# Performance work log

Measured on AMD Instinct MI355X. Metric: run time of the kernel, lower is better.

Reference implementation:

```python
import jax, jax.numpy as jnp
import numpy as np

MP_TIMES = 3  # mp_times from init


def setup_inputs() -> dict:
    key = jax.random.key(0)
    ks = jax.random.split(key, 16)
    N, E, F, EF = 10000, 50000, 32, 16
    DL, D, G, GD, OUT = 128, 64, 256, 8, 1

    def w(k, shape, fan_in):
        return jax.random.normal(k, shape, jnp.float32) / np.float32(np.sqrt(fan_in))

    return {
        "x": jax.random.normal(ks[0], (N, F), jnp.float32),
        "edge_index": jax.random.randint(ks[1], (2, E), 0, N),
        "edge_attr": jax.random.uniform(ks[2], (E, EF), jnp.float32),
        "batch": jax.random.randint(ks[3], (N,), 0, G),
        "graph_attr": jax.random.normal(ks[4], (G, GD), jnp.float32),
        # lin0
        "W0": w(ks[5], (D, F), F), "b0": jnp.zeros((D,), jnp.float32),
        # edge network MLP: EF -> DL -> D*D
        "We1": w(ks[6], (DL, EF), EF), "be1": jnp.zeros((DL,), jnp.float32),
        "We2": w(ks[7], (D * D, DL), DL), "be2": jnp.zeros((D * D,), jnp.float32),
        # NNConv root weight + bias
        "Wroot": w(ks[8], (D, D), D), "bconv": jnp.zeros((D,), jnp.float32),
        # GRU (torch gate order: r, z, n)
        "W_ih": w(ks[9], (3 * D, D), D), "W_hh": w(ks[10], (3 * D, D), D),
        "b_ih": jnp.zeros((3 * D,), jnp.float32), "b_hh": jnp.zeros((3 * D,), jnp.float32),
        # lin1 takes cat(node_state, graph_attr) -> D  (sized D+GD to make the source's cat runnable)
        "W1": w(ks[11], (D, D + GD), D + GD), "b1": jnp.zeros((D,), jnp.float32),
        # lin2
        "W2": w(ks[12], (OUT, D), D), "b2": jnp.zeros((OUT,), jnp.float32),
    }


def reference(x, edge_index, edge_attr, batch, graph_attr,
              W0, b0, We1, be1, We2, be2, Wroot, bconv,
              W_ih, W_hh, b_ih, b_hh, W1, b1, W2, b2):
    N = x.shape[0]
    D = W0.shape[0]
    src, dst = edge_index[0], edge_index[1]

    # Per-edge weight matrices from the edge MLP (loop-invariant: edge_attr is constant).
    ew = jnp.maximum(edge_attr @ We1.T + be1, 0.0) @ We2.T + be2  # [E, D*D]
    ew = ew.reshape(-1, D, D)                                      # [E, D, D]

    # mean-aggregation denominator (isolated nodes keep 0 via max(deg,1))
    deg = jax.ops.segment_sum(jnp.ones(src.shape[0], jnp.float32), dst, num_segments=N)
    denom = jnp.maximum(deg, 1.0)[:, None]                         # [N, 1]

    out = jnp.maximum(x @ W0.T + b0, 0.0)                          # [N, D]
    h = out
    for _ in range(MP_TIMES):
        # NNConv: gather -> per-edge matmul -> scatter-mean, plus root transform
        msg = jnp.einsum('ei,eio->eo', out[src], ew)               # [E, D]
        agg = jax.ops.segment_sum(msg, dst, num_segments=N) / denom
        m = jnp.maximum(agg + out @ Wroot.T + bconv, 0.0)          # [N, D]
        # single GRU step (torch GRUCell math, gate order r,z,n)
        gi = m @ W_ih.T + b_ih
        gh = h @ W_hh.T + b_hh
        i_r, i_z, i_n = jnp.split(gi, 3, axis=-1)
        h_r, h_z, h_n = jnp.split(gh, 3, axis=-1)
        r = jax.nn.sigmoid(i_r + h_r)
        z = jax.nn.sigmoid(i_z + h_z)
        n = jnp.tanh(i_n + r * h_n)
        h = (1.0 - z) * n + z * h
        out = h

    cat = jnp.concatenate([out, graph_attr[batch]], axis=-1)       # [N, D+GD]
    hid = jnp.maximum(cat @ W1.T + b1, 0.0)
    return hid @ W2.T + b2                                         # [N, dim_output]
```

## Files before the change

kernel.cpp:

```cpp
#include <hip/hip_runtime.h>
#include <hip/hip_bf16.h>
#include <math.h>

#define FIN 32
#define EFD 16
#define GDIM 8
#define ISPLIT 2

typedef __attribute__((ext_vector_type(8))) short short8;
typedef __attribute__((ext_vector_type(4))) float f32x4;

static __device__ __forceinline__ float bf2f(unsigned short u) {
  return __uint_as_float(((unsigned)u) << 16);
}
static __device__ __forceinline__ unsigned short f2bf(float f) {
  unsigned u = __float_as_uint(f);
  unsigned r = (u + 0x7FFFu + ((u >> 16) & 1u)) >> 16;
  return (unsigned short)r;
}

__global__ void zero_f32(float* __restrict__ p, int n) {
  int i = blockIdx.x * blockDim.x + threadIdx.x;
  if (i < n) p[i] = 0.0f;
}

__global__ void deg_kernel(const int* __restrict__ dst, float* __restrict__ deg, int E) {
  int e = blockIdx.x * blockDim.x + threadIdx.x;
  if (e < E) atomicAdd(&deg[dst[e]], 1.0f);
}

__global__ void setup_fused(const float* __restrict__ ea, const float* __restrict__ We1,
                            const float* __restrict__ be1, unsigned short* __restrict__ hidden,
                            const float* __restrict__ We2, unsigned short* __restrict__ We2f,
                            const float* __restrict__ Wroot, const float* __restrict__ W_hh,
                            const float* __restrict__ be2, const float* __restrict__ W_ih,
                            unsigned short* __restrict__ Wc_fh, unsigned short* __restrict__ Wc_fl,
                            unsigned short* __restrict__ Wih_fh, unsigned short* __restrict__ Wih_fl,
                            const float* __restrict__ x, const float* __restrict__ W0,
                            const float* __restrict__ b0, float* __restrict__ state,
                            int E, int N, int eB, int cB, int pB) {
  int b = blockIdx.x;
  if (b < eB) {
    int idx = b * 256 + threadIdx.x;
    int e = idx >> 7, l = idx & 127;
    if (e >= E) return;
    float acc = be1[l];
    const float* er = ea + (size_t)e * EFD;
    const float* wr = We1 + (size_t)l * EFD;
    #pragma unroll
    for (int j = 0; j < EFD; ++j) acc += er[j] * wr[j];
    hidden[idx] = f2bf(fmaxf(acc, 0.0f));
    return;
  }
  b -= eB;
  if (b < cB) {
    int fidx = b * 256 + threadIdx.x;
    if (fidx >= 4096 * 128) return;
    int j    = fidx & 7;
    int lane = (fidx >> 3) & 63;
    int kk   = (fidx >> 9) & 3;
    int wave = (fidx >> 11) & 3;
    int i    = fidx >> 13;
    int quad = lane >> 4, col = lane & 15;
    int row  = i * 64 + wave * 16 + col;
    int cw   = kk * 32 + quad * 8 + j;
    We2f[fidx] = f2bf(We2[(size_t)row * 128 + cw]);
    return;
  }
  b -= cB;
  if (b < pB) {
    int idx = b * 256 + threadIdx.x;
    if (idx >= 20480 + 12288) return;
    if (idx < 20480) {
      int j = idx & 7, lane = (idx >> 3) & 63, kk = (idx >> 9) & 1, cgk = idx >> 10;
      int quad = lane >> 4, mcol = lane & 15;
      int wave = cgk / 5, cg = cgk % 5;
      int c = wave * 80 + cg * 16 + mcol;
      int cw = kk * 32 + quad * 8 + j;
      float w;
      if (c < 64)       w = Wroot[c * 64 + cw];
      else if (c < 256) w = W_hh[(c - 64) * 64 + cw];
      else              w = be2[cw * 64 + (c - 256)];
      unsigned short h = f2bf(w);
      Wc_fh[idx] = h;
      Wc_fl[idx] = f2bf(w - bf2f(h));
    } else {
      int t = idx - 20480;
      int j = t & 7, lane = (t >> 3) & 63, kk = (t >> 9) & 1, gw = t >> 10;
      int quad = lane >> 4, mcol = lane & 15;
      int g = gw >> 2, wave = gw & 3;
      int row = g * 64 + wave * 16 + mcol;
      int cw = kk * 32 + quad * 8 + j;
      float w = W_ih[row * 64 + cw];
      unsigned short h = f2bf(w);
      Wih_fh[t] = h;
      Wih_fl[t] = f2bf(w - bf2f(h));
    }
    return;
  }
  b -= pB;
  {
    int idx = b * 256 + threadIdx.x;
    int n = idx >> 6, d = idx & 63;
    if (n >= N) return;
    float acc = b0[d];
    const float* xr = x + (size_t)n * FIN;
    const float* wr = W0 + (size_t)d * FIN;
    #pragma unroll
    for (int f = 0; f < FIN; ++f) acc += xr[f] * wr[f];
    state[idx] = fmaxf(acc, 0.0f);
  }
}

#define MFMA(A, B, C) __builtin_amdgcn_mfma_f32_16x16x32_bf16((A), (B), (C), 0, 0, 0)

__global__ __launch_bounds__(256) void pre_kernel(const float* __restrict__ state,
    const unsigned short* __restrict__ Wc_fh, const unsigned short* __restrict__ Wc_fl,
    float* __restrict__ R, int N) {
  __shared__ __align__(16) unsigned short Sh[32 * 72], Sl[32 * 72];
  int tid = threadIdx.x;
  int n0 = blockIdx.x * 32;
  {
    int nl = tid >> 3, part = tid & 7;
    int gn = n0 + nl;
    const float* sp = state + (size_t)gn * 64 + part * 8;
    #pragma unroll
    for (int j = 0; j < 2; ++j) {
      float4 v = make_float4(0.f, 0.f, 0.f, 0.f);
      if (gn < N) v = *(const float4*)(sp + j * 4);
      int base = nl * 72 + part * 8 + j * 4;
      unsigned short h;
      h = f2bf(v.x); Sh[base + 0] = h; Sl[base + 0] = f2bf(v.x - bf2f(h));
      h = f2bf(v.y); Sh[base + 1] = h; Sl[base + 1] = f2bf(v.y - bf2f(h));
      h = f2bf(v.z); Sh[base + 2] = h; Sl[base + 2] = f2bf(v.z - bf2f(h));
      h = f2bf(v.w); Sh[base + 3] = h; Sl[base + 3] = f2bf(v.w - bf2f(h));
    }
  }
  __syncthreads();
  int lane = tid & 63, wave = tid >> 6;
  int quad = lane >> 4, mcol = lane & 15;
  short8 ah[2][2], al[2][2];
  #pragma unroll
  for (int mt = 0; mt < 2; ++mt)
    #pragma unroll
    for (int kk = 0; kk < 2; ++kk) {
      ah[mt][kk] = *(const short8*)&Sh[(mt * 16 + mcol) * 72 + kk * 32 + quad * 8];
      al[mt][kk] = *(const short8*)&Sl[(mt * 16 + mcol) * 72 + kk * 32 + quad * 8];
    }
  int c0w = wave * 80;
  #pragma unroll 1
  for (int cg = 0; cg < 5; ++cg) {
    int c = c0w + cg * 16 + mcol;
    const unsigned short* bhp = Wc_fh + (size_t)(wave * 5 + cg) * 1024 + lane * 8;
    const unsigned short* blp = Wc_fl + (size_t)(wave * 5 + cg) * 1024 + lane * 8;
    short8 bh0 = *(const short8*)bhp, bh1 = *(const short8*)(bhp + 512);
    short8 bl0 = *(const short8*)blp, bl1 = *(const short8*)(blp + 512);
    #pragma unroll
    for (int mt = 0; mt < 2; ++mt) {
      f32x4 p = (f32x4){0.f, 0.f, 0.f, 0.f};
      p = MFMA(al[mt][0], bh0, p);
      p = MFMA(ah[mt][0], bl0, p);
      p = MFMA(ah[mt][0], bh0, p);
      p = MFMA(al[mt][1], bh1, p);
      p = MFMA(ah[mt][1], bl1, p);
      p = MFMA(ah[mt][1], bh1, p);
      #pragma unroll
      for (int r = 0; r < 4; ++r) {
        int row = n0 + mt * 16 + quad * 4 + r;
        if (row < N) R[(size_t)row * 320 + c] = p[r];
      }
    }
  }
}

__global__ __launch_bounds__(256) void msg_fused(const int* __restrict__ ei,
    const float* __restrict__ state, const unsigned short* __restrict__ hidden,
    const unsigned short* __restrict__ We2f, const float* __restrict__ R,
    float* __restrict__ agg, int E) {
  __shared__ __align__(16) char smem[64 * 136 * 2];
  __shared__ int srcs[64], dsts[64];
  unsigned short* Hs = (unsigned short*)smem;
  float* St = (float*)smem;
  int tid = threadIdx.x;
  int e0 = blockIdx.x * 64;
  int i0 = blockIdx.y * 32;
  if (tid < 64) {
    int e = e0 + tid;
    srcs[tid] = (e < E) ? ei[e] : -1;
    dsts[tid] = (e < E) ? ei[E + e] : -1;
  }
  {
    int er = tid >> 2, part = tid & 3;
    int ge = e0 + er;
    const unsigned short* hp = hidden + (size_t)ge * 128 + part * 32;
    #pragma unroll
    for (int j = 0; j < 4; ++j) {
      uint4 v = make_uint4(0u, 0u, 0u, 0u);
      if (ge < E) v = *(const uint4*)(hp + j * 8);
      *(uint4*)&Hs[er * 136 + part * 32 + j * 8] = v;
    }
  }
  __syncthreads();
  int lane = tid & 63, wave = tid >> 6;
  int n0 = wave * 16;
  int quad = lane >> 4, col = lane & 15;
  short8 a[4][4];
  #pragma unroll
  for (int mt = 0; mt < 4; ++mt)
    #pragma unroll
    for (int kk = 0; kk < 4; ++kk)
      a[mt][kk] = *(const short8*)&Hs[(mt * 16 + col) * 136 + kk * 32 + quad * 8];
  float4 sreg[2];
  {
    int sn = srcs[lane];
    const float* sp = state + (size_t)(sn < 0 ? 0 : sn) * 64 + i0 + wave * 8;
    #pragma unroll
    for (int j = 0; j < 2; ++j) {
      float4 v = make_float4(0.f, 0.f, 0.f, 0.f);
      if (sn >= 0) v = *(const float4*)(sp + j * 4);
      sreg[j] = v;
    }
  }
  __syncthreads();
  #pragma unroll
  for (int j = 0; j < 2; ++j) {
    int i = wave * 8 + j * 4;
    St[(i + 0) * 64 + lane] = sreg[j].x;
    St[(i + 1) * 64 + lane] = sreg[j].y;
    St[(i + 2) * 64 + lane] = sreg[j].z;
    St[(i + 3) * 64 + lane] = sreg[j].w;
  }
  __syncthreads();

  f32x4 macc0 = (f32x4){0.f,0.f,0.f,0.f}, macc1 = (f32x4){0.f,0.f,0.f,0.f};
  f32x4 macc2 = (f32x4){0.f,0.f,0.f,0.f}, macc3 = (f32x4){0.f,0.f,0.f,0.f};
  const unsigned short* bptr = We2f + (size_t)i0 * 8192 + wave * 2048 + lane * 8;
  short8 Xa = *(const short8*)(bptr + 0);
  short8 Xb = *(const short8*)(bptr + 512);
  short8 Xc = *(const short8*)(bptr + 1024);
  short8 Xd = *(const short8*)(bptr + 1536);
  short8 Ya, Yb, Yc, Yd;
  #pragma unroll 1
  for (int ii = 0; ii < 16; ++ii) {
    int i = ii * 2;
    {
      const unsigned short* bn = bptr + (size_t)(i + 1) * 8192;
      Ya = *(const short8*)(bn + 0);
      Yb = *(const short8*)(bn + 512);
      Yc = *(const short8*)(bn + 1024);
      Yd = *(const short8*)(bn + 1536);
    }
    {
      f32x4 sv0 = *(const f32x4*)&St[i * 64 +  0 + quad * 4];
      f32x4 sv1 = *(const f32x4*)&St[i * 64 + 16 + quad * 4];
      f32x4 sv2 = *(const f32x4*)&St[i * 64 + 32 + quad * 4];
      f32x4 sv3 = *(const f32x4*)&St[i * 64 + 48 + quad * 4];
      f32x4 p0 = (f32x4){0.f,0.f,0.f,0.f}, p1 = (f32x4){0.f,0.f,0.f,0.f};
      f32x4 p2 = (f32x4){0.f,0.f,0.f,0.f}, p3 = (f32x4){0.f,0.f,0.f,0.f};
      p0 = MFMA(a[0][0], Xa, p0); p1 = MFMA(a[1][0], Xa, p1);
      p2 = MFMA(a[2][0], Xa, p2); p3 = MFMA(a[3][0], Xa, p3);
      p0 = MFMA(a[0][1], Xb, p0); p1 = MFMA(a[1][1], Xb, p1);
      p2 = MFMA(a[2][1], Xb, p2); p3 = MFMA(a[3][1], Xb, p3);
      p0 = MFMA(a[0][2], Xc, p0); p1 = MFMA(a[1][2], Xc, p1);
      p2 = MFMA(a[2][2], Xc, p2); p3 = MFMA(a[3][2], Xc, p3);
      p0 = MFMA(a[0][3], Xd, p0); p1 = MFMA(a[1][3], Xd, p1);
      p2 = MFMA(a[2][3], Xd, p2); p3 = MFMA(a[3][3], Xd, p3);
      macc0 += sv0 * p0; macc1 += sv1 * p1; macc2 += sv2 * p2; macc3 += sv3 * p3;
    }
    if (ii < 15) {
      const unsigned short* bn = bptr + (size_t)(i + 2) * 8192;
      Xa = *(const short8*)(bn + 0);
      Xb = *(const short8*)(bn + 512);
      Xc = *(const short8*)(bn + 1024);
      Xd = *(const short8*)(bn + 1536);
    }
    {
      int io = i + 1;
      f32x4 sv0 = *(const f32x4*)&St[io * 64 +  0 + quad * 4];
      f32x4 sv1 = *(const f32x4*)&St[io * 64 + 16 + quad * 4];
      f32x4 sv2 = *(const f32x4*)&St[io * 64 + 32 + quad * 4];
      f32x4 sv3 = *(const f32x4*)&St[io * 64 + 48 + quad * 4];
      f32x4 p0 = (f32x4){0.f,0.f,0.f,0.f}, p1 = (f32x4){0.f,0.f,0.f,0.f};
      f32x4 p2 = (f32x4){0.f,0.f,0.f,0.f}, p3 = (f32x4){0.f,0.f,0.f,0.f};
      p0 = MFMA(a[0][0], Ya, p0); p1 = MFMA(a[1][0], Ya, p1);
      p2 = MFMA(a[2][0], Ya, p2); p3 = MFMA(a[3][0], Ya, p3);
      p0 = MFMA(a[0][1], Yb, p0); p1 = MFMA(a[1][1], Yb, p1);
      p2 = MFMA(a[2][1], Yb, p2); p3 = MFMA(a[3][1], Yb, p3);
      p0 = MFMA(a[0][2], Yc, p0); p1 = MFMA(a[1][2], Yc, p1);
      p2 = MFMA(a[2][2], Yc, p2); p3 = MFMA(a[3][2], Yc, p3);
      p0 = MFMA(a[0][3], Yd, p0); p1 = MFMA(a[1][3], Yd, p1);
      p2 = MFMA(a[2][3], Yd, p2); p3 = MFMA(a[3][3], Yd, p3);
      macc0 += sv0 * p0; macc1 += sv1 * p1; macc2 += sv2 * p2; macc3 += sv3 * p3;
    }
  }
  int addu = (blockIdx.y == 0);
  f32x4 maccA[4] = {macc0, macc1, macc2, macc3};
  #pragma unroll
  for (int mt = 0; mt < 4; ++mt) {
    #pragma unroll
    for (int r = 0; r < 4; ++r) {
      int el = mt * 16 + quad * 4 + r;
      int d = dsts[el];
      if (d >= 0) {
        float val = maccA[mt][r];
        if (addu) val += R[(size_t)srcs[el] * 320 + 256 + n0 + col];
        atomicAdd(&agg[(size_t)d * 64 + n0 + col], val);
      }
    }
  }
}

__global__ __launch_bounds__(256) void gate_pre(float* __restrict__ agg,
    const float* __restrict__ deg, float* __restrict__ state,
    float* __restrict__ R, const float* __restrict__ bconv,
    const unsigned short* __restrict__ Wih_fh, const unsigned short* __restrict__ Wih_fl,
    const float* __restrict__ b_ih, const float* __restrict__ b_hh,
    const unsigned short* __restrict__ Wc_fh, const unsigned short* __restrict__ Wc_fl,
    int N, int do_pre) {
  __shared__ __align__(16) unsigned short Mh[16 * 72], Ml[16 * 72];
  int tid = threadIdx.x;
  int n0 = blockIdx.x * 16;
  {
    int nl = tid >> 4, part = tid & 15;
    int gn = n0 + nl;
    float inv = 1.0f;
    if (gn < N) inv = 1.0f / fmaxf(deg[gn], 1.0f);
    int o = part * 4;
    float4 av = make_float4(0.f, 0.f, 0.f, 0.f);
    float4 rv = make_float4(0.f, 0.f, 0.f, 0.f);
    if (gn < N) {
      av = *(const float4*)(agg + (size_t)gn * 64 + o);
      rv = *(const float4*)(R + (size_t)gn * 320 + o);
    }
    float4 bv = *(const float4*)(bconv + o);
    float m0 = fmaxf(av.x * inv + rv.x + bv.x, 0.0f);
    float m1 = fmaxf(av.y * inv + rv.y + bv.y, 0.0f);
    float m2 = fmaxf(av.z * inv + rv.z + bv.z, 0.0f);
    float m3 = fmaxf(av.w * inv + rv.w + bv.w, 0.0f);
    int base = nl * 72 + o;
    unsigned short h;
    h = f2bf(m0); Mh[base + 0] = h; Ml[base + 0] = f2bf(m0 - bf2f(h));
    h = f2bf(m1); Mh[base + 1] = h; Ml[base + 1] = f2bf(m1 - bf2f(h));
    h = f2bf(m2); Mh[base + 2] = h; Ml[base + 2] = f2bf(m2 - bf2f(h));
    h = f2bf(m3); Mh[base + 3] = h; Ml[base + 3] = f2bf(m3 - bf2f(h));
    if (gn < N)
      *(float4*)(agg + (size_t)gn * 64 + o) = make_float4(0.f, 0.f, 0.f, 0.f);
  }
  __syncthreads();
  int lane = tid & 63, wave = tid >> 6;
  int quad = lane >> 4, mcol = lane & 15;
  short8 ah[2], al[2];
  #pragma unroll
  for (int kk = 0; kk < 2; ++kk) {
    ah[kk] = *(const short8*)&Mh[mcol * 72 + kk * 32 + quad * 8];
    al[kk] = *(const short8*)&Ml[mcol * 72 + kk * 32 + quad * 8];
  }
  int c = wave * 16 + mcol;
  f32x4 accg[3];
  #pragma unroll 1
  for (int g = 0; g < 3; ++g) {
    const unsigned short* bhp = Wih_fh + (size_t)g * 4096 + wave * 1024 + lane * 8;
    const unsigned short* blp = Wih_fl + (size_t)g * 4096 + wave * 1024 + lane * 8;
    short8 bh0 = *(const short8*)bhp, bh1 = *(const short8*)(bhp + 512);
    short8 bl0 = *(const short8*)blp, bl1 = *(const short8*)(blp + 512);
    f32x4 p = (f32x4){0.f, 0.f, 0.f, 0.f};
    p = MFMA(al[0], bh0, p);
    p = MFMA(ah[0], bl0, p);
    p = MFMA(ah[0], bh0, p);
    p = MFMA(al[1], bh1, p);
    p = MFMA(ah[1], bl1, p);
    p = MFMA(ah[1], bh1, p);
    accg[g] = p;
  }
  float bir = b_ih[c], biz = b_ih[64 + c], bin = b_ih[128 + c];
  float bhr = b_hh[c], bhz = b_hh[64 + c], bhn = b_hh[128 + c];
  float hnew[4];
  #pragma unroll
  for (int r = 0; r < 4; ++r) {
    int node = n0 + quad * 4 + r;
    hnew[r] = 0.0f;
    if (node >= N) continue;
    const float* Rn = R + (size_t)node * 320;
    float gir = accg[0][r] + bir + Rn[64 + c] + bhr;
    float giz = accg[1][r] + biz + Rn[128 + c] + bhz;
    float ghn = Rn[192 + c] + bhn;
    float rg = 1.0f / (1.0f + expf(-gir));
    float zg = 1.0f / (1.0f + expf(-giz));
    float ng = tanhf(accg[2][r] + bin + rg * ghn);
    size_t si = (size_t)node * 64 + c;
    float h = state[si];
    float hv = (1.0f - zg) * ng + zg * h;
    state[si] = hv;
    hnew[r] = hv;
  }
  if (!do_pre) return;
  __syncthreads();
  #pragma unroll
  for (int r = 0; r < 4; ++r) {
    int base = (quad * 4 + r) * 72 + c;
    float v = hnew[r];
    unsigned short h = f2bf(v);
    Mh[base] = h; Ml[base] = f2bf(v - bf2f(h));
  }
  __syncthreads();
  short8 ph[2], pl[2];
  #pragma unroll
  for (int kk = 0; kk < 2; ++kk) {
    ph[kk] = *(const short8*)&Mh[mcol * 72 + kk * 32 + quad * 8];
    pl[kk] = *(const short8*)&Ml[mcol * 72 + kk * 32 + quad * 8];
  }
  #pragma unroll 1
  for (int cg = 0; cg < 5; ++cg) {
    int cc = wave * 80 + cg * 16 + mcol;
    const unsigned short* bhp = Wc_fh + (size_t)(wave * 5 + cg) * 1024 + lane * 8;
    const unsigned short* blp = Wc_fl + (size_t)(wave * 5 + cg) * 1024 + lane * 8;
    short8 bh0 = *(const short8*)bhp, bh1 = *(const short8*)(bhp + 512);
    short8 bl0 = *(const short8*)blp, bl1 = *(const short8*)(blp + 512);
    f32x4 p = (f32x4){0.f, 0.f, 0.f, 0.f};
    p = MFMA(pl[0], bh0, p);
    p = MFMA(ph[0], bl0, p);
    p = MFMA(ph[0], bh0, p);
    p = MFMA(pl[1], bh1, p);
    p = MFMA(ph[1], bl1, p);
    p = MFMA(ph[1], bh1, p);
    #pragma unroll
    for (int r = 0; r < 4; ++r) {
      int row = n0 + quad * 4 + r;
      if (row < N) R[(size_t)row * 320 + cc] = p[r];
    }
  }
}

__global__ __launch_bounds__(256) void final_kernel(const float* __restrict__ state,
    const int* __restrict__ batch, const float* __restrict__ gattr,
    const float* __restrict__ W1, const float* __restrict__ b1,
    const float* __restrict__ W2, const float* __restrict__ b2,
    float* __restrict__ out, int N) {
  int lane = threadIdx.x & 63;
  int n = blockIdx.x * 4 + (threadIdx.x >> 6);
  if (n >= N) return;
  float s = state[(size_t)n * 64 + lane];
  int b = batch[n];
  float acc = b1[lane];
  const float* w = W1 + (size_t)lane * 72;
  for (int i = 0; i < 64; ++i) acc += __shfl(s, i) * w[i];
  const float* gar = gattr + (size_t)b * GDIM;
  #pragma unroll
  for (int j = 0; j < GDIM; ++j) acc += gar[j] * w[64 + j];
  float hid = fmaxf(acc, 0.0f);
  float v = hid * W2[lane];
  #pragma unroll
  for (int off = 32; off > 0; off >>= 1) v += __shfl_xor(v, off);
  if (lane == 0) out[n] = v + b2[0];
}

extern "C" void kernel_launch(void* const* d_in, const int* in_sizes, int n_in,
                              void* d_out, int out_size, void* d_ws, size_t ws_size,
                              hipStream_t stream) {
  const float* x     = (const float*)d_in[0];
  const int*   ei    = (const int*)d_in[1];
  const float* ea    = (const float*)d_in[2];
  const int*   batch = (const int*)d_in[3];
  const float* ga    = (const float*)d_in[4];
  const float* W0    = (const float*)d_in[5];
  const float* b0    = (const float*)d_in[6];
  const float* We1   = (const float*)d_in[7];
  const float* be1   = (const float*)d_in[8];
  const float* We2   = (const float*)d_in[9];
  const float* be2   = (const float*)d_in[10];
  const float* Wroot = (const float*)d_in[11];
  const float* bconv = (const float*)d_in[12];
  const float* W_ih  = (const float*)d_in[13];
  const float* W_hh  = (const float*)d_in[14];
  const float* b_ih  = (const float*)d_in[15];
  const float* b_hh  = (const float*)d_in[16];
  const float* W1    = (const float*)d_in[17];
  const float* b1    = (const float*)d_in[18];
  const float* W2    = (const float*)d_in[19];
  const float* b2    = (const float*)d_in[20];
  int N = in_sizes[0] / FIN;
  int E = in_sizes[1] / 2;
  float* out = (float*)d_out;

  char* p = (char*)d_ws;
  float* state = (float*)p; p += (size_t)N * 64 * 4;
  float* agg   = (float*)p; p += (size_t)N * 64 * 4;
  float* deg   = (float*)p; p += ((size_t)N * 4 + 15) & ~(size_t)15;
  float* R     = (float*)p; p += (size_t)N * 320 * 4;
  unsigned short* hidden = (unsigned short*)p; p += (size_t)E * 128 * 2;
  unsigned short* We2f   = (unsigned short*)p; p += (size_t)4096 * 128 * 2;
  unsigned short* Wc_fh  = (unsigned short*)p; p += 320 * 64 * 2;
  unsigned short* Wc_fl  = (unsigned short*)p; p += 320 * 64 * 2;
  unsigned short* Wih_fh = (unsigned short*)p; p += 192 * 64 * 2;
  unsigned short* Wih_fl = (unsigned short*)p; p += 192 * 64 * 2;

  int tileBlocks32 = (N + 31) / 32;
  int tileBlocks16 = (N + 15) / 16;
  int edgeBlocks = (E + 63) / 64;

  int eB = (E * 128 + 255) / 256;
  int cB = (4096 * 128 + 255) / 256;
  int pB = (32768 + 255) / 256;
  int lB = (N * 64 + 255) / 256;

  zero_f32<<<(N * 65 + 255) / 256, 256, 0, stream>>>(agg, N * 65);
  deg_kernel<<<(E + 255) / 256, 256, 0, stream>>>(ei + E, deg, E);
  setup_fused<<<eB + cB + pB + lB, 256, 0, stream>>>(
      ea, We1, be1, hidden, We2, We2f, Wroot, W_hh, be2, W_ih,
      Wc_fh, Wc_fl, Wih_fh, Wih_fl, x, W0, b0, state, E, N, eB, cB, pB);
  pre_kernel<<<tileBlocks32, 256, 0, stream>>>(state, Wc_fh, Wc_fl, R, N);
  for (int t = 0; t < 3; ++t) {
    dim3 mg(edgeBlocks, ISPLIT);
    msg_fused<<<mg, 256, 0, stream>>>(ei, state, hidden, We2f, R, agg, E);
    gate_pre<<<tileBlocks16, 256, 0, stream>>>(agg, deg, state, R, bconv,
                                               Wih_fh, Wih_fl, b_ih, b_hh,
                                               Wc_fh, Wc_fl, N, (t < 2) ? 1 : 0);
  }
  final_kernel<<<(N + 3) / 4, 256, 0, stream>>>(state, batch, ga, W1, b1, W2, b2, out, N);
}
```

Before: 409.5 us.

## Split bias-term scatter into separate blocks and fuse final MLP into last gate kernel

The per-edge addition of the R[src] slice (the extra column block at offset 256) moves out of the MFMA message blocks into extra lightweight blocks in the same launch, one wave per edge, each doing a coalesced 64-lane atomic scatter. The 2D grid is flattened to 1D. The final readout MLP (lin1 + lin2) is folded into the last gate_pre launch, which removes one kernel launch and a re-read of state. The price is more atomic traffic, since the bias term now gets its own atomics per edge, and a serial per-wave loop over 4 nodes in the fused tail.

```diff
diff --git a/kernel.cpp b/kernel.cpp
--- a/kernel.cpp
+++ b/kernel.cpp
@@ -176,18 +176,32 @@
 __global__ __launch_bounds__(256) void msg_fused(const int* __restrict__ ei,
     const float* __restrict__ state, const unsigned short* __restrict__ hidden,
     const unsigned short* __restrict__ We2f, const float* __restrict__ R,
-    float* __restrict__ agg, int E) {
+    float* __restrict__ agg, int E, int edgeBlocks) {
+  int tid = threadIdx.x;
+  int lane = tid & 63, wave = tid >> 6;
+  int mb = edgeBlocks * ISPLIT;
+  if ((int)blockIdx.x >= mb) {
+    int e = (blockIdx.x - mb) * 4 + wave;
+    if (e < E) {
+      int src = ei[e], dst = ei[E + e];
+      float val = R[(size_t)src * 320 + 256 + lane];
+      atomicAdd(&agg[(size_t)dst * 64 + lane], val);
+    }
+    return;
+  }
   __shared__ __align__(16) char smem[64 * 136 * 2];
-  __shared__ int srcs[64], dsts[64];
+  __shared__ int dsts[64];
   unsigned short* Hs = (unsigned short*)smem;
   float* St = (float*)smem;
-  int tid = threadIdx.x;
-  int e0 = blockIdx.x * 64;
-  int i0 = blockIdx.y * 32;
-  if (tid < 64) {
-    int e = e0 + tid;
-    srcs[tid] = (e < E) ? ei[e] : -1;
-    dsts[tid] = (e < E) ? ei[E + e] : -1;
+  int by = blockIdx.x / edgeBlocks;
+  int bx = blockIdx.x % edgeBlocks;
+  int e0 = bx * 64;
+  int i0 = by * 32;
+  int snL;
+  {
+    int eL = e0 + lane;
+    snL = (eL < E) ? ei[eL] : -1;
+    if (tid < 64) dsts[tid] = (eL < E) ? ei[E + eL] : -1;
   }
   {
     int er = tid >> 2, part = tid & 3;
@@ -201,7 +215,6 @@
     }
   }
   __syncthreads();
-  int lane = tid & 63, wave = tid >> 6;
   int n0 = wave * 16;
   int quad = lane >> 4, col = lane & 15;
   short8 a[4][4];
@@ -212,12 +225,11 @@
       a[mt][kk] = *(const short8*)&Hs[(mt * 16 + col) * 136 + kk * 32 + quad * 8];
   float4 sreg[2];
   {
-    int sn = srcs[lane];
-    const float* sp = state + (size_t)(sn < 0 ? 0 : sn) * 64 + i0 + wave * 8;
+    const float* sp = state + (size_t)(snL < 0 ? 0 : snL) * 64 + i0 + wave * 8;
     #pragma unroll
     for (int j = 0; j < 2; ++j) {
       float4 v = make_float4(0.f, 0.f, 0.f, 0.f);
-      if (sn >= 0) v = *(const float4*)(sp + j * 4);
+      if (snL >= 0) v = *(const float4*)(sp + j * 4);
       sreg[j] = v;
     }
   }
@@ -293,7 +305,6 @@
       macc0 += sv0 * p0; macc1 += sv1 * p1; macc2 += sv2 * p2; macc3 += sv3 * p3;
     }
   }
-  int addu = (blockIdx.y == 0);
   f32x4 maccA[4] = {macc0, macc1, macc2, macc3};
   #pragma unroll
   for (int mt = 0; mt < 4; ++mt) {
@@ -301,11 +312,8 @@
     for (int r = 0; r < 4; ++r) {
       int el = mt * 16 + quad * 4 + r;
       int d = dsts[el];
-      if (d >= 0) {
-        float val = maccA[mt][r];
-        if (addu) val += R[(size_t)srcs[el] * 320 + 256 + n0 + col];
-        atomicAdd(&agg[(size_t)d * 64 + n0 + col], val);
-      }
+      if (d >= 0)
+        atomicAdd(&agg[(size_t)d * 64 + n0 + col], maccA[mt][r]);
     }
   }
 }
@@ -316,7 +324,10 @@
     const unsigned short* __restrict__ Wih_fh, const unsigned short* __restrict__ Wih_fl,
     const float* __restrict__ b_ih, const float* __restrict__ b_hh,
     const unsigned short* __restrict__ Wc_fh, const unsigned short* __restrict__ Wc_fl,
-    int N, int do_pre) {
+    const int* __restrict__ batch, const float* __restrict__ gattr,
+    const float* __restrict__ W1, const float* __restrict__ b1,
+    const float* __restrict__ W2, const float* __restrict__ b2,
+    float* __restrict__ out, int N, int do_pre) {
   __shared__ __align__(16) unsigned short Mh[16 * 72], Ml[16 * 72];
   int tid = threadIdx.x;
   int n0 = blockIdx.x * 16;
@@ -393,65 +404,69 @@
     state[si] = hv;
     hnew[r] = hv;
   }
-  if (!do_pre) return;
-  __syncthreads();
-  #pragma unroll
-  for (int r = 0; r < 4; ++r) {
-    int base = (quad * 4 + r) * 72 + c;
-    float v = hnew[r];
-    unsigned short h = f2bf(v);
-    Mh[base] = h; Ml[base] = f2bf(v - bf2f(h));
-  }
-  __syncthreads();
-  short8 ph[2], pl[2];
-  #pragma unroll
-  for (int kk = 0; kk < 2; ++kk) {
-    ph[kk] = *(const short8*)&Mh[mcol * 72 + kk * 32 + quad * 8];
-    pl[kk] = *(const short8*)&Ml[mcol * 72 + kk * 32 + quad * 8];
-  }
-  #pragma unroll 1
-  for (int cg = 0; cg < 5; ++cg) {
-    int cc = wave * 80 + cg * 16 + mcol;
-    const unsigned short* bhp = Wc_fh + (size_t)(wave * 5 + cg) * 1024 + lane * 8;
-    const unsigned short* blp = Wc_fl + (size_t)(wave * 5 + cg) * 1024 + lane * 8;
-    short8 bh0 = *(const short8*)bhp, bh1 = *(const short8*)(bhp + 512);
-    short8 bl0 = *(const short8*)blp, bl1 = *(const short8*)(blp + 512);
-    f32x4 p = (f32x4){0.f, 0.f, 0.f, 0.f};
-    p = MFMA(pl[0], bh0, p);
-    p = MFMA(ph[0], bl0, p);
-    p = MFMA(ph[0], bh0, p);
-    p = MFMA(pl[1], bh1, p);
-    p = MFMA(ph[1], bl1, p);
-    p = MFMA(ph[1], bh1, p);
+  if (do_pre) {
+    __syncthreads();
     #pragma unroll
     for (int r = 0; r < 4; ++r) {
-      int row = n0 + quad * 4 + r;
-      if (row < N) R[(size_t)row * 320 + cc] = p[r];
-    }
-  }
-}
-
-__global__ __launch_bounds__(256) void final_kernel(const float* __restrict__ state,
-    const int* __restrict__ batch, const float* __restrict__ gattr,
-    const float* __restrict__ W1, const float* __restrict__ b1,
-    const float* __restrict__ W2, const float* __restrict__ b2,
-    float* __restrict__ out, int N) {
-  int lane = threadIdx.x & 63;
-  int n = blockIdx.x * 4 + (threadIdx.x >> 6);
-  if (n >= N) return;
-  float s = state[(size_t)n * 64 + lane];
-  int b = batch[n];
-  float acc = b1[lane];
-  const float* w = W1 + (size_t)lane * 72;
-  for (int i = 0; i < 64; ++i) acc += __shfl(s, i) * w[i];
-  const float* gar = gattr + (size_t)b * GDIM;
-  #pragma unroll
-  for (int j = 0; j < GDIM; ++j) acc += gar[j] * w[64 + j];
-  float hid = fmaxf(acc, 0.0f);
-  float v = hid * W2[lane];
-  #pragma unroll
-  for (int off = 32; off > 0; off >>= 1) v += __shfl_xor(v, off);
-  if (lane == 0) out[n] = v + b2[0];
+      int base = (quad * 4 + r) * 72 + c;
+      float v = hnew[r];
+      unsigned short h = f2bf(v);
+      Mh[base] = h; Ml[base] = f2bf(v - bf2f(h));
+    }
+    __syncthreads();
+    short8 ph[2], pl[2];
+    #pragma unroll
+    for (int kk = 0; kk < 2; ++kk) {
+      ph[kk] = *(const short8*)&Mh[mcol * 72 + kk * 32 + quad * 8];
+      pl[kk] = *(const short8*)&Ml[mcol * 72 + kk * 32 + quad * 8];
+    }
+    #pragma unroll 1
+    for (int cg = 0; cg < 5; ++cg) {
+      int cc = wave * 80 + cg * 16 + mcol;
+      const unsigned short* bhp = Wc_fh + (size_t)(wave * 5 + cg) * 1024 + lane * 8;
+      const unsigned short* blp = Wc_fl + (size_t)(wave * 5 + cg) * 1024 + lane * 8;
+      short8 bh0 = *(const short8*)bhp, bh1 = *(const short8*)(bhp + 512);
+      short8 bl0 = *(const short8*)blp, bl1 = *(const short8*)(blp + 512);
+      f32x4 p = (f32x4){0.f, 0.f, 0.f, 0.f};
+      p = MFMA(pl[0], bh0, p);
+      p = MFMA(ph[0], bl0, p);
+      p = MFMA(ph[0], bh0, p);
+      p = MFMA(pl[1], bh1, p);
+      p = MFMA(ph[1], bl1, p);
+      p = MFMA(ph[1], bh1, p);
+      #pragma unroll
+      for (int r = 0; r < 4; ++r) {
+        int row = n0 + quad * 4 + r;
+        if (row < N) R[(size_t)row * 320 + cc] = p[r];
+      }
+    }
+  } else {
+    __syncthreads();
+    float* Hf = (float*)Mh;
+    #pragma unroll
+    for (int r = 0; r < 4; ++r)
+      Hf[(quad * 4 + r) * 64 + c] = hnew[r];
+    __syncthreads();
+    const float* w = W1 + (size_t)lane * 72;
+    #pragma unroll 1
+    for (int nl = 0; nl < 4; ++nl) {
+      int node_local = wave * 4 + nl;
+      int node = n0 + node_local;
+      if (node >= N) continue;
+      float s = Hf[node_local * 64 + lane];
+      int b = batch[node];
+      float acc = b1[lane];
+      for (int i = 0; i < 64; ++i) acc += __shfl(s, i) * w[i];
+      const float* gar = gattr + (size_t)b * GDIM;
+      #pragma unroll
+      for (int j = 0; j < GDIM; ++j) acc += gar[j] * w[64 + j];
+      float hid = fmaxf(acc, 0.0f);
+      float v = hid * W2[lane];
+      #pragma unroll
+      for (int off = 32; off > 0; off >>= 1) v += __shfl_xor(v, off);
+      if (lane == 0) out[node] = v + b2[0];
+    }
+  }
 }
 
 extern "C" void kernel_launch(void* const* d_in, const int* in_sizes, int n_in,
@@ -497,6 +512,7 @@
   int tileBlocks32 = (N + 31) / 32;
   int tileBlocks16 = (N + 15) / 16;
   int edgeBlocks = (E + 63) / 64;
+  int uBlocks = (E + 3) / 4;
 
   int eB = (E * 128 + 255) / 256;
   int cB = (4096 * 128 + 255) / 256;
@@ -510,11 +526,12 @@
       Wc_fh, Wc_fl, Wih_fh, Wih_fl, x, W0, b0, state, E, N, eB, cB, pB);
   pre_kernel<<<tileBlocks32, 256, 0, stream>>>(state, Wc_fh, Wc_fl, R, N);
   for (int t = 0; t < 3; ++t) {
-    dim3 mg(edgeBlocks, ISPLIT);
-    msg_fused<<<mg, 256, 0, stream>>>(ei, state, hidden, We2f, R, agg, E);
+    msg_fused<<<edgeBlocks * ISPLIT + uBlocks, 256, 0, stream>>>(
+        ei, state, hidden, We2f, R, agg, E, edgeBlocks);
     gate_pre<<<tileBlocks16, 256, 0, stream>>>(agg, deg, state, R, bconv,
                                                Wih_fh, Wih_fl, b_ih, b_hh,
-                                               Wc_fh, Wc_fl, N, (t < 2) ? 1 : 0);
-  }
-  final_kernel<<<(N + 3) / 4, 256, 0, stream>>>(state, batch, ga, W1, b1, W2, b2, out, N);
-}
+                                               Wc_fh, Wc_fl, batch, ga,
+                                               W1, b1, W2, b2, out,
+                                               N, (t < 2) ? 1 : 0);
+  }
+}
```

Measured after the change: 446.0 us. 1.09x slower.
